# Optimization experiments

Hardware: AMD Instinct MI355X
Metric: run time of the kernel (lower is better)

The kernel has to match this reference:

```python
import jax, jax.numpy as jnp
import numpy as np


def setup_inputs() -> dict:
    key = jax.random.key(0)
    k1, k2 = jax.random.split(key)
    B, D, H, W = 64, 64, 32, 32
    K = 1024
    z_e = jax.random.normal(k1, (B, D, H, W), dtype=jnp.float32)
    embedding = jax.random.normal(k2, (K, D), dtype=jnp.float32)
    return {"z_e": z_e, "embedding": embedding}


def reference(z_e, embedding):
    # Eval-mode forward of VectorQuantizer (EMA buffer updates are training-only state).
    B, D, H, W = z_e.shape
    K = embedding.shape[0]
    # (N, D) flattened encoder outputs, N = B*H*W
    flat = jnp.transpose(z_e, (0, 2, 3, 1)).reshape(-1, D)
    dist = (jnp.sum(flat * flat, axis=1, keepdims=True)
            + jnp.sum(embedding * embedding, axis=1)
            - 2.0 * flat @ embedding.T)  # (N, K)
    indices = jnp.argmin(dist, axis=1)  # (N,)
    z_q_flat = embedding[indices]  # (N, D) gather
    z_q = jnp.transpose(z_q_flat.reshape(B, H, W, D), (0, 3, 1, 2))
    # commitment loss: mse(z_e, sg(z_q))
    commitment_loss = jnp.mean((z_e - jax.lax.stop_gradient(z_q)) ** 2)
    # straight-through estimator
    z_q = z_e + jax.lax.stop_gradient(z_q - z_e)
    indices_bhw = indices.reshape(B, H, W)
    # fraction of codebook entries used this batch (jit-friendly unique count)
    used = jnp.zeros((K,), dtype=jnp.float32).at[indices].set(1.0)
    codebook_usage = jnp.sum(used) / K
    return z_q, commitment_loss, indices_bhw, codebook_usage
```

## Files before the change

### kernel.cpp

```cpp
#include <hip/hip_runtime.h>


#define DIMS 64
#define K_CODES 1024
#define N_QUERIES 65536
#define HW 1024
#define TOTAL_ELEMS 4194304
#define PLANE 4096

typedef __attribute__((ext_vector_type(8))) short v8s;
typedef __attribute__((ext_vector_type(4))) float f32x4;

__device__ inline unsigned short f2bf(float x) {
    union { float f; unsigned u; } v; v.f = x;
    unsigned r = v.u + 0x7fff + ((v.u >> 16) & 1);
    return (unsigned short)(r >> 16);
}
__device__ inline float bf2f(unsigned short h) {
    union { unsigned u; float f; } v; v.u = ((unsigned)h) << 16; return v.f;
}

__global__ void vq_prep(const float* __restrict__ emb, float* __restrict__ ws_norm,
                        int* __restrict__ ws_flags, float* __restrict__ ws_loss) {
    int k = blockIdx.x * 256 + threadIdx.x;
    const float4* row = (const float4*)(emb + k * DIMS);
    float s = 0.f;
#pragma unroll
    for (int i = 0; i < 16; ++i) {
        float4 v = row[i];
        s += v.x * v.x + v.y * v.y + v.z * v.z + v.w * v.w;
    }
    ws_norm[k] = s;
    ws_flags[k] = 0;
    if (k == 0) *ws_loss = 0.f;
}

#define MFMA16(A_, B_, C_) __builtin_amdgcn_mfma_f32_16x16x32_bf16(A_, B_, C_, 0, 0, 0)

__global__ __launch_bounds__(256, 2)
void vq_main(const float* __restrict__ z_e, const float* __restrict__ emb,
             const float* __restrict__ ws_norm, int* __restrict__ ws_flags,
             float* __restrict__ ws_loss, float* __restrict__ out) {
    __shared__ unsigned short ldsB[2][3 * PLANE];
    __shared__ int   fIdx[128];
    __shared__ float wsum[4];

    const int tid  = threadIdx.x;
    const int lane = tid & 63;
    const int wid  = tid >> 6;
    const int qbase = blockIdx.x * 128;
    const int b    = qbase >> 10;
    const int hwb  = qbase & (HW - 1);

    const int col  = lane & 15;
    const int qd   = lane >> 4;

    v8s afr[2][2][3];
    {
        const float* zb = z_e + b * (DIMS * HW);
#pragma unroll
        for (int rt = 0; rt < 2; ++rt) {
            int hwq = hwb + wid * 32 + rt * 16 + col;
#pragma unroll
            for (int kc = 0; kc < 2; ++kc) {
                int dbase = kc * 32 + qd * 8;
#pragma unroll
                for (int j = 0; j < 8; ++j) {
                    float x = zb[(dbase + j) * HW + hwq];
                    unsigned short h = f2bf(x);  float r1 = x - bf2f(h);
                    unsigned short m = f2bf(r1); float r2 = r1 - bf2f(m);
                    afr[rt][kc][0][j] = (short)h;
                    afr[rt][kc][1][j] = (short)m;
                    afr[rt][kc][2][j] = (short)f2bf(r2);
                }
            }
        }
    }

    float bestv[2][4];
    int   besti[2][4];
#pragma unroll
    for (int rt = 0; rt < 2; ++rt)
#pragma unroll
        for (int r = 0; r < 4; ++r) { bestv[rt][r] = 3.4e38f; besti[rt][r] = 0; }

    float4 regs[4];

    auto stage_loads = [&](int t) {
        const float4* src = (const float4*)(emb + t * 64 * DIMS);
#pragma unroll
        for (int i = 0; i < 4; ++i) regs[i] = src[tid + 256 * i];
    };
    auto stage_write = [&](int bb) {
        unsigned short* dst = &ldsB[bb][0];
#pragma unroll
        for (int i = 0; i < 4; ++i) {
            int e    = (tid + 256 * i) * 4;
            int code = e >> 6;
            int d    = e & 63;
            int o    = d >> 3;
            int sub  = d & 7;
            float xs[4] = {regs[i].x, regs[i].y, regs[i].z, regs[i].w};
            unsigned short h[4], mm_[4], l[4];
#pragma unroll
            for (int q = 0; q < 4; ++q) {
                float x = xs[q];
                unsigned short hh = f2bf(x);  float r1 = x - bf2f(hh);
                unsigned short mh = f2bf(r1); float r2 = r1 - bf2f(mh);
                h[q] = hh; mm_[q] = mh; l[q] = f2bf(r2);
            }
            int base = (o * 64 + (code ^ (o << 1))) * 8 + sub;
            uint2 uh, um, ul;
            uh.x = (unsigned)h[0]   | ((unsigned)h[1] << 16);
            uh.y = (unsigned)h[2]   | ((unsigned)h[3] << 16);
            um.x = (unsigned)mm_[0] | ((unsigned)mm_[1] << 16);
            um.y = (unsigned)mm_[2] | ((unsigned)mm_[3] << 16);
            ul.x = (unsigned)l[0]   | ((unsigned)l[1] << 16);
            ul.y = (unsigned)l[2]   | ((unsigned)l[3] << 16);
            *(uint2*)(dst + base)             = uh;
            *(uint2*)(dst + PLANE + base)     = um;
            *(uint2*)(dst + 2 * PLANE + base) = ul;
        }
    };

    stage_loads(0);
    stage_write(0);
    __syncthreads();

    for (int t = 0; t < 16; ++t) {
        const int cur = t & 1;
        if (t < 15) stage_loads(t + 1);
        const unsigned short* bufc = &ldsB[cur][0];
#pragma unroll
        for (int cs = 0; cs < 4; ++cs) {
            float nrm = ws_norm[t * 64 + cs * 16 + col];
            v8s bfr[2][3];
#pragma unroll
            for (int kc = 0; kc < 2; ++kc) {
                int oct  = kc * 4 + qd;
                int slot = (cs * 16 + col) ^ (oct << 1);
#pragma unroll
                for (int p = 0; p < 3; ++p)
                    bfr[kc][p] = *(const v8s*)(bufc + p * PLANE + (oct * 64 + slot) * 8);
            }
            f32x4 acc0 = {0.f, 0.f, 0.f, 0.f};
            f32x4 acc1 = {0.f, 0.f, 0.f, 0.f};
#pragma unroll
            for (int kc = 0; kc < 2; ++kc) {
                acc0 = MFMA16(afr[0][kc][0], bfr[kc][0], acc0);
                acc1 = MFMA16(afr[1][kc][0], bfr[kc][0], acc1);
                acc0 = MFMA16(afr[0][kc][0], bfr[kc][1], acc0);
                acc1 = MFMA16(afr[1][kc][0], bfr[kc][1], acc1);
                acc0 = MFMA16(afr[0][kc][1], bfr[kc][0], acc0);
                acc1 = MFMA16(afr[1][kc][1], bfr[kc][0], acc1);
                acc0 = MFMA16(afr[0][kc][1], bfr[kc][1], acc0);
                acc1 = MFMA16(afr[1][kc][1], bfr[kc][1], acc1);
                acc0 = MFMA16(afr[0][kc][0], bfr[kc][2], acc0);
                acc1 = MFMA16(afr[1][kc][0], bfr[kc][2], acc1);
                acc0 = MFMA16(afr[0][kc][2], bfr[kc][0], acc0);
                acc1 = MFMA16(afr[1][kc][2], bfr[kc][0], acc1);
            }
            int cbase = t * 64 + cs * 16 + col;
#pragma unroll
            for (int r = 0; r < 4; ++r) {
                float d0 = fmaf(-2.f, acc0[r], nrm);
                if (d0 < bestv[0][r]) { bestv[0][r] = d0; besti[0][r] = cbase; }
                float d1 = fmaf(-2.f, acc1[r], nrm);
                if (d1 < bestv[1][r]) { bestv[1][r] = d1; besti[1][r] = cbase; }
            }
        }
        if (t < 15) stage_write(1 - cur);
        __syncthreads();
    }

#pragma unroll
    for (int rt = 0; rt < 2; ++rt)
#pragma unroll
    for (int r = 0; r < 4; ++r) {
        float v = bestv[rt][r];
        int   idx = besti[rt][r];
#pragma unroll
        for (int m = 8; m >= 1; m >>= 1) {
            float ov = __shfl_xor(v, m, 64);
            int   oi = __shfl_xor(idx, m, 64);
            if (ov < v || (ov == v && oi < idx)) { v = ov; idx = oi; }
        }
        if (col == 0) {
            int q = wid * 32 + rt * 16 + qd * 4 + r;
            fIdx[q] = idx;
            out[TOTAL_ELEMS + 1 + qbase + q] = (float)idx;
            ws_flags[idx] = 1;
        }
    }
    __syncthreads();

    const int q  = tid & 127;
    const int dh = tid >> 7;
    const int n  = qbase + q;
    const int bb = n >> 10;
    const int hw = n & (HW - 1);
    const int myIdx = fIdx[q];
    const float* erow = emb + myIdx * DIMS;
    float lsum = 0.f;
#pragma unroll
    for (int it = 0; it < 32; ++it) {
        int d = it * 2 + dh;
        float v = erow[d];
        int   o = bb * (DIMS * HW) + d * HW + hw;
        float ze = z_e[o];
        out[o] = v;
        float df = ze - v;
        lsum = fmaf(df, df, lsum);
    }
#pragma unroll
    for (int off = 32; off > 0; off >>= 1) lsum += __shfl_down(lsum, off, 64);
    if (lane == 0) wsum[wid] = lsum;
    __syncthreads();
    if (tid == 0) atomicAdd(ws_loss, wsum[0] + wsum[1] + wsum[2] + wsum[3]);
}

__global__ void vq_final(const int* __restrict__ flags, const float* __restrict__ loss,
                         float* __restrict__ out) {
    __shared__ int cnt[256];
    int tid = threadIdx.x;
    int c = flags[tid] + flags[tid + 256] + flags[tid + 512] + flags[tid + 768];
    cnt[tid] = c;
    __syncthreads();
    for (int s = 128; s > 0; s >>= 1) {
        if (tid < s) cnt[tid] += cnt[tid + s];
        __syncthreads();
    }
    if (tid == 0) {
        out[TOTAL_ELEMS] = *loss / (float)TOTAL_ELEMS;
        out[TOTAL_ELEMS + 1 + N_QUERIES] = (float)cnt[0] / (float)K_CODES;
    }
}

extern "C" void kernel_launch(void* const* d_in, const int* in_sizes, int n_in,
                              void* d_out, int out_size, void* d_ws, size_t ws_size,
                              hipStream_t stream) {
    const float* z_e = (const float*)d_in[0];
    const float* emb = (const float*)d_in[1];
    float* out = (float*)d_out;
    float* ws_norm  = (float*)d_ws;
    int*   ws_flags = (int*)((char*)d_ws + 4096);
    float* ws_loss  = (float*)((char*)d_ws + 8192);

    vq_prep<<<4, 256, 0, stream>>>(emb, ws_norm, ws_flags, ws_loss);
    vq_main<<<512, 256, 0, stream>>>(z_e, emb, ws_norm, ws_flags, ws_loss, out);
    vq_final<<<1, 256, 0, stream>>>(ws_flags, ws_loss, out);
}
```

Baseline: 136.5 us.

## Switch distance GEMM from 16x16x32 to 32x32x16 bf16 MFMA tiles

Replaces the 16x16x32 MFMA tiling with 32x32x16 MFMAs. Each wave now computes a 32-query by 32-code tile, using two accumulators that split the K dimension so independent MFMA chains can interleave. It also restructures the A/B fragment layouts, the argmin bookkeeping (16 results per lane), and the cross-lane reduction and index mapping to match. The goal is fewer MFMA issues and fewer LDS fragment reads per unit of work. In exchange it adds accumulator register pressure and a longer per-instruction latency.

```diff
diff --git a/kernel.cpp b/kernel.cpp
--- a/kernel.cpp
+++ b/kernel.cpp
@@ -9,7 +9,7 @@
 #define PLANE 4096
 
 typedef __attribute__((ext_vector_type(8))) short v8s;
-typedef __attribute__((ext_vector_type(4))) float f32x4;
+typedef __attribute__((ext_vector_type(16))) float f32x16;
 
 __device__ inline unsigned short f2bf(float x) {
     union { float f; unsigned u; } v; v.f = x;
@@ -35,7 +35,7 @@
     if (k == 0) *ws_loss = 0.f;
 }
 
-#define MFMA16(A_, B_, C_) __builtin_amdgcn_mfma_f32_16x16x32_bf16(A_, B_, C_, 0, 0, 0)
+#define MFMA32(A_, B_, C_) __builtin_amdgcn_mfma_f32_32x32x16_bf16(A_, B_, C_, 0, 0, 0)
 
 __global__ __launch_bounds__(256, 2)
 void vq_main(const float* __restrict__ z_e, const float* __restrict__ emb,
@@ -52,37 +52,32 @@
     const int b    = qbase >> 10;
     const int hwb  = qbase & (HW - 1);
 
-    const int col  = lane & 15;
-    const int qd   = lane >> 4;
-
-    v8s afr[2][2][3];
+    const int l31 = lane & 31;
+    const int kh  = lane >> 5;
+
+    v8s afr[4][3];
     {
         const float* zb = z_e + b * (DIMS * HW);
-#pragma unroll
-        for (int rt = 0; rt < 2; ++rt) {
-            int hwq = hwb + wid * 32 + rt * 16 + col;
-#pragma unroll
-            for (int kc = 0; kc < 2; ++kc) {
-                int dbase = kc * 32 + qd * 8;
-#pragma unroll
-                for (int j = 0; j < 8; ++j) {
-                    float x = zb[(dbase + j) * HW + hwq];
-                    unsigned short h = f2bf(x);  float r1 = x - bf2f(h);
-                    unsigned short m = f2bf(r1); float r2 = r1 - bf2f(m);
-                    afr[rt][kc][0][j] = (short)h;
-                    afr[rt][kc][1][j] = (short)m;
-                    afr[rt][kc][2][j] = (short)f2bf(r2);
-                }
-            }
-        }
-    }
-
-    float bestv[2][4];
-    int   besti[2][4];
-#pragma unroll
-    for (int rt = 0; rt < 2; ++rt)
-#pragma unroll
-        for (int r = 0; r < 4; ++r) { bestv[rt][r] = 3.4e38f; besti[rt][r] = 0; }
+        const int hwq = hwb + wid * 32 + l31;
+#pragma unroll
+        for (int kk = 0; kk < 4; ++kk) {
+            int dbase = kk * 16 + kh * 8;
+#pragma unroll
+            for (int j = 0; j < 8; ++j) {
+                float x = zb[(dbase + j) * HW + hwq];
+                unsigned short h = f2bf(x);  float r1 = x - bf2f(h);
+                unsigned short m = f2bf(r1); float r2 = r1 - bf2f(m);
+                afr[kk][0][j] = (short)h;
+                afr[kk][1][j] = (short)m;
+                afr[kk][2][j] = (short)f2bf(r2);
+            }
+        }
+    }
+
+    float bestv[16];
+    int   besti[16];
+#pragma unroll
+    for (int r = 0; r < 16; ++r) { bestv[r] = 3.4e38f; besti[r] = 0; }
 
     float4 regs[4];
 
@@ -132,41 +127,39 @@
         if (t < 15) stage_loads(t + 1);
         const unsigned short* bufc = &ldsB[cur][0];
 #pragma unroll
-        for (int cs = 0; cs < 4; ++cs) {
-            float nrm = ws_norm[t * 64 + cs * 16 + col];
-            v8s bfr[2][3];
-#pragma unroll
-            for (int kc = 0; kc < 2; ++kc) {
-                int oct  = kc * 4 + qd;
-                int slot = (cs * 16 + col) ^ (oct << 1);
+        for (int cg = 0; cg < 2; ++cg) {
+            const int ccol = cg * 32 + l31;
+            float nrm = ws_norm[t * 64 + ccol];
+            v8s bfr[4][3];
+#pragma unroll
+            for (int kk = 0; kk < 4; ++kk) {
+                int o    = kk * 2 + kh;
+                int slot = ccol ^ (o << 1);
 #pragma unroll
                 for (int p = 0; p < 3; ++p)
-                    bfr[kc][p] = *(const v8s*)(bufc + p * PLANE + (oct * 64 + slot) * 8);
-            }
-            f32x4 acc0 = {0.f, 0.f, 0.f, 0.f};
-            f32x4 acc1 = {0.f, 0.f, 0.f, 0.f};
-#pragma unroll
-            for (int kc = 0; kc < 2; ++kc) {
-                acc0 = MFMA16(afr[0][kc][0], bfr[kc][0], acc0);
-                acc1 = MFMA16(afr[1][kc][0], bfr[kc][0], acc1);
-                acc0 = MFMA16(afr[0][kc][0], bfr[kc][1], acc0);
-                acc1 = MFMA16(afr[1][kc][0], bfr[kc][1], acc1);
-                acc0 = MFMA16(afr[0][kc][1], bfr[kc][0], acc0);
-                acc1 = MFMA16(afr[1][kc][1], bfr[kc][0], acc1);
-                acc0 = MFMA16(afr[0][kc][1], bfr[kc][1], acc0);
-                acc1 = MFMA16(afr[1][kc][1], bfr[kc][1], acc1);
-                acc0 = MFMA16(afr[0][kc][0], bfr[kc][2], acc0);
-                acc1 = MFMA16(afr[1][kc][0], bfr[kc][2], acc1);
-                acc0 = MFMA16(afr[0][kc][2], bfr[kc][0], acc0);
-                acc1 = MFMA16(afr[1][kc][2], bfr[kc][0], acc1);
-            }
-            int cbase = t * 64 + cs * 16 + col;
-#pragma unroll
-            for (int r = 0; r < 4; ++r) {
-                float d0 = fmaf(-2.f, acc0[r], nrm);
-                if (d0 < bestv[0][r]) { bestv[0][r] = d0; besti[0][r] = cbase; }
-                float d1 = fmaf(-2.f, acc1[r], nrm);
-                if (d1 < bestv[1][r]) { bestv[1][r] = d1; besti[1][r] = cbase; }
+                    bfr[kk][p] = *(const v8s*)(bufc + p * PLANE + (o * 64 + slot) * 8);
+            }
+            f32x16 aP = {0.f}, aQ = {0.f};
+#pragma unroll
+            for (int kk = 0; kk < 2; ++kk) {
+                aP = MFMA32(afr[kk][0], bfr[kk][0], aP);
+                aQ = MFMA32(afr[kk + 2][0], bfr[kk + 2][0], aQ);
+                aP = MFMA32(afr[kk][0], bfr[kk][1], aP);
+                aQ = MFMA32(afr[kk + 2][0], bfr[kk + 2][1], aQ);
+                aP = MFMA32(afr[kk][1], bfr[kk][0], aP);
+                aQ = MFMA32(afr[kk + 2][1], bfr[kk + 2][0], aQ);
+                aP = MFMA32(afr[kk][1], bfr[kk][1], aP);
+                aQ = MFMA32(afr[kk + 2][1], bfr[kk + 2][1], aQ);
+                aP = MFMA32(afr[kk][0], bfr[kk][2], aP);
+                aQ = MFMA32(afr[kk + 2][0], bfr[kk + 2][2], aQ);
+                aP = MFMA32(afr[kk][2], bfr[kk][0], aP);
+                aQ = MFMA32(afr[kk + 2][2], bfr[kk + 2][0], aQ);
+            }
+            int cbase = t * 64 + ccol;
+#pragma unroll
+            for (int r = 0; r < 16; ++r) {
+                float dd = fmaf(-2.f, aQ[r], fmaf(-2.f, aP[r], nrm));
+                if (dd < bestv[r]) { bestv[r] = dd; besti[r] = cbase; }
             }
         }
         if (t < 15) stage_write(1 - cur);
@@ -174,19 +167,17 @@
     }
 
 #pragma unroll
-    for (int rt = 0; rt < 2; ++rt)
-#pragma unroll
-    for (int r = 0; r < 4; ++r) {
-        float v = bestv[rt][r];
-        int   idx = besti[rt][r];
-#pragma unroll
-        for (int m = 8; m >= 1; m >>= 1) {
+    for (int r = 0; r < 16; ++r) {
+        float v = bestv[r];
+        int   idx = besti[r];
+#pragma unroll
+        for (int m = 16; m >= 1; m >>= 1) {
             float ov = __shfl_xor(v, m, 64);
             int   oi = __shfl_xor(idx, m, 64);
             if (ov < v || (ov == v && oi < idx)) { v = ov; idx = oi; }
         }
-        if (col == 0) {
-            int q = wid * 32 + rt * 16 + qd * 4 + r;
+        if (l31 == 0) {
+            int q = wid * 32 + (r & 3) + 8 * (r >> 2) + 4 * kh;
             fIdx[q] = idx;
             out[TOTAL_ELEMS + 1 + qbase + q] = (float)idx;
             ws_flags[idx] = 1;
```

Result: no change. 138.7 us (+1.5%).
